# Performance work log

Hardware: AMD Instinct MI355X
Metric: run time of the kernel (lower is better)

Reference implementation:

```python
import jax, jax.numpy as jnp
import numpy as np

B, S, K = 256, 50, 8
D, NH, NL = 512, 8, 2
N_KNOWS, N_PROBS = 1000, 20000
L2 = 2 * NL  # forward layers then backward layers, stacked
HD = D // NH
NEG = -1e9


def _ln(x, g, b, eps=1e-5):
    mu = x.mean(-1, keepdims=True)
    v = ((x - mu) ** 2).mean(-1, keepdims=True)
    return (x - mu) * jax.lax.rsqrt(v + eps) * g + b


def _block(x, m, Wq, bq, Wk, bk, Wv, bv, g1, be1, W1, b1, W2, b2, g2, be2):
    # x: [3B,S,D], m: [3B,1,S,S] additive-OR mask (True = blocked)
    Bx, Sx, Dx = x.shape
    Q = (x @ Wq + bq).reshape(Bx, Sx, NH, HD)
    Kt = (x @ Wk + bk).reshape(Bx, Sx, NH, HD)
    V = (x @ Wv + bv).reshape(Bx, Sx, NH, HD)
    a = jnp.einsum('bqnh,bknh->bnqk', Q, Kt) * (HD ** -0.5)
    a = jnp.where(m, NEG, a)
    p = jax.nn.softmax(a, axis=-1)
    p = jnp.where(m, 0.0, p)  # masked_fill + softmax + where, as in torch source
    o = jnp.einsum('bnqk,bknh->bqnh', p, V).reshape(Bx, Sx, Dx)
    x = _ln(x + o, g1, be1)
    h = jnp.maximum(x @ W1 + b1, 0.0) @ W2 + b2
    return _ln(x + h, g2, be2)


def _forward(probs_his, knows_his, corrs_his, knows_tab, probs_tab, types_tab, pos_tab,
             Wq, bq, Wk, bk, Wv, bv, g1, be1, W1, b1, W2, b2, g2, be2,
             pW1, pb1, pW2, pb2, pW3, pb3):
    info = knows_tab[knows_his].sum(-2) + probs_tab[probs_his] + pos_tab[jnp.arange(S)][None]
    c = corrs_his
    right_t = jnp.where(c, 1, 2)   # corrs==False -> 2
    wrong_t = jnp.where(c, 2, 0)   # corrs==True  -> 2
    norm_t = c.astype(jnp.int32)
    # fold the 3 counterfactual passes (right / wrong / normal) into the batch dim
    x3 = jnp.concatenate([info + types_tab[right_t], info + types_tab[wrong_t], info + types_tab[norm_t]], 0)
    kpm = jnp.tile(probs_his == 0, (3, 1))               # key padding mask [3B,S]
    km = kpm[:, :, None] | kpm[:, None, :]               # OR-combined [3B,S,S]
    tri = jnp.triu(jnp.ones((S, S), bool), 1)
    fm = (tri[None] | km)[:, None]                       # forward (causal) mask
    bm = (tri.T[None] | km)[:, None]                     # backward (anti-causal) mask
    f = x3
    b = x3
    for i in range(NL):
        f = _block(f, fm, Wq[i], bq[i], Wk[i], bk[i], Wv[i], bv[i], g1[i], be1[i], W1[i], b1[i], W2[i], b2[i], g2[i], be2[i])
    for i in range(NL, L2):
        b = _block(b, bm, Wq[i], bq[i], Wk[i], bk[i], Wv[i], bv[i], g1[i], be1[i], W1[i], b1[i], W2[i], b2[i], g2[i], be2[i])
    out = jnp.concatenate([b[:, :1], f[:, :-2] + b[:, 2:], f[:, -1:]], 1)
    h = jnp.concatenate([out, jnp.tile(info, (3, 1, 1))], -1)
    h = jnp.maximum(h @ pW1 + pb1, 0.0)
    h = jnp.maximum(h @ pW2 + pb2, 0.0)
    sc = jax.nn.sigmoid((h @ pW3 + pb3)[..., 0]).reshape(3, B, S)
    # zero out padded positions instead of ragged boolean gather (fixed shape, jit-safe)
    return jnp.where((probs_his > 0)[None], sc, 0.0)


def setup_inputs() -> dict:
    key = jax.random.key(0)
    ks = jax.random.split(key, 16)
    sc = 0.02
    d = {}
    d['probs_his'] = jax.random.randint(ks[0], (B, S), 0, N_PROBS)
    d['knows_his'] = jax.random.randint(ks[1], (B, S, K), 0, N_KNOWS + 1)
    d['corrs_his'] = jax.random.randint(ks[2], (B, S), 0, 2).astype(bool)
    d['knows_tab'] = (jax.random.normal(ks[3], (N_KNOWS + 1, D)) * sc).at[0].set(0.0)  # padding_idx=0
    d['probs_tab'] = (jax.random.normal(ks[4], (N_PROBS + 1, D)) * sc).at[0].set(0.0)
    d['types_tab'] = jax.random.normal(ks[5], (3, D)) * sc
    d['pos_tab'] = jax.random.normal(ks[6], (50, D)) * sc
    d['Wq'] = jax.random.normal(ks[7], (L2, D, D)) * sc
    d['Wk'] = jax.random.normal(ks[8], (L2, D, D)) * sc
    d['Wv'] = jax.random.normal(ks[9], (L2, D, D)) * sc
    d['W1'] = jax.random.normal(ks[10], (L2, D, D)) * sc
    d['W2'] = jax.random.normal(ks[11], (L2, D, D)) * sc
    for n in ('bq', 'bk', 'bv', 'b1', 'b2', 'be1', 'be2'):
        d[n] = jnp.zeros((L2, D))
    d['g1'] = jnp.ones((L2, D))
    d['g2'] = jnp.ones((L2, D))
    d['pW1'] = jax.random.normal(ks[12], (2 * D, D)) * sc
    d['pb1'] = jnp.zeros((D,))
    d['pW2'] = jax.random.normal(ks[13], (D, D // 2)) * sc
    d['pb2'] = jnp.zeros((D // 2,))
    d['pW3'] = jax.random.normal(ks[14], (D // 2, 1)) * sc
    d['pb3'] = jnp.zeros((1,))
    return d


def reference(probs_his, knows_his, corrs_his, knows_tab, probs_tab, types_tab, pos_tab,
              Wq, bq, Wk, bk, Wv, bv, g1, be1, W1, b1, W2, b2, g2, be2,
              pW1, pb1, pW2, pb2, pW3, pb3):
    return _forward(probs_his, knows_his, corrs_his, knows_tab, probs_tab, types_tab, pos_tab,
                    Wq, bq, Wk, bk, Wv, bv, g1, be1, W1, b1, W2, b2, g2, be2,
                    pW1, pb1, pW2, pb2, pW3, pb3)
```

## Files before the change

### kernel.cpp

```cpp
#include <hip/hip_runtime.h>
#include <hip/hip_bf16.h>

#define SEQ 50
#define DD  512
#define NHD 8
#define HDIM 64
#define MPROWS 38400
#define MTROWS 76800

typedef __hip_bfloat16 bf;
typedef __attribute__((ext_vector_type(8))) short bf16x8;
typedef __attribute__((ext_vector_type(4))) float f32x4;

__device__ __forceinline__ float bf2f(unsigned short u) {
    unsigned int x = ((unsigned int)u) << 16;
    return __builtin_bit_cast(float, x);
}
__device__ __forceinline__ unsigned short f2bu(float f) {
    unsigned int u = __builtin_bit_cast(unsigned int, f);
    u += 0x7fffu + ((u >> 16) & 1u);
    return (unsigned short)(u >> 16);
}

#define ASYNC16(g, l) __builtin_amdgcn_global_load_lds( \
    (__attribute__((address_space(1))) void*)(g),       \
    (__attribute__((address_space(3))) void*)(l), 16, 0, 0)

__global__ __launch_bounds__(256) void transpose_cast(
    const float* __restrict__ src, bf* __restrict__ dst,
    int R, int C, size_t sStride, size_t dStride)
{
    __shared__ float tile[32][33];
    int l = blockIdx.z;
    src += (size_t)l * sStride;
    dst += (size_t)l * dStride;
    int c0 = blockIdx.x * 32, r0 = blockIdx.y * 32;
    int tx = threadIdx.x & 31, ty = threadIdx.x >> 5;
    for (int i = ty; i < 32; i += 8)
        tile[i][tx] = src[(size_t)(r0 + i) * C + c0 + tx];
    __syncthreads();
    for (int i = ty; i < 32; i += 8)
        dst[(size_t)(c0 + i) * R + r0 + tx] = __float2bfloat16(tile[tx][i]);
}

__global__ __launch_bounds__(256) void biascat_kernel(
    const float* __restrict__ bq, const float* __restrict__ bk,
    const float* __restrict__ bv, float* __restrict__ out)
{
    int i = blockIdx.x * 256 + threadIdx.x;
    if (i >= 4 * 1536) return;
    int l = i / 1536, c = i % 1536;
    float v;
    if (c < 512)       v = bq[l * 512 + c];
    else if (c < 1024) v = bk[l * 512 + c - 512];
    else               v = bv[l * 512 + c - 1024];
    out[i] = v;
}

__global__ __launch_bounds__(256) void embed_kernel(
    const int* __restrict__ probs_his, const int* __restrict__ knows_his,
    const int* __restrict__ corrs, const float* __restrict__ knows_tab,
    const float* __restrict__ probs_tab, const float* __restrict__ types_tab,
    const float* __restrict__ pos_tab, bf* __restrict__ info, bf* __restrict__ X)
{
    int bs = blockIdx.x * 4 + (threadIdx.x >> 6);
    int lane = threadIdx.x & 63;
    int s = bs % SEQ;
    int p = probs_his[bs];
    int c = corrs[bs];
    int d0 = lane * 8;

    float v[8];
    #pragma unroll
    for (int j = 0; j < 8; ++j)
        v[j] = probs_tab[(size_t)p * DD + d0 + j] + pos_tab[(size_t)s * DD + d0 + j];
    for (int k = 0; k < 8; ++k) {
        int ki = knows_his[bs * 8 + k];
        const float* kr = knows_tab + (size_t)ki * DD + d0;
        #pragma unroll
        for (int j = 0; j < 8; ++j) v[j] += kr[j];
    }
    int t0 = c ? 1 : 2;
    int t1 = c ? 2 : 0;
    int t2 = c ? 1 : 0;
    const float* T0 = types_tab + t0 * DD + d0;
    const float* T1 = types_tab + t1 * DD + d0;
    const float* T2 = types_tab + t2 * DD + d0;
    uint4 xi, x0, x1, x2;
    unsigned short* pi = (unsigned short*)&xi;
    unsigned short* p0 = (unsigned short*)&x0;
    unsigned short* p1 = (unsigned short*)&x1;
    unsigned short* p2 = (unsigned short*)&x2;
    #pragma unroll
    for (int j = 0; j < 8; ++j) {
        pi[j] = f2bu(v[j]);
        p0[j] = f2bu(v[j] + T0[j]);
        p1[j] = f2bu(v[j] + T1[j]);
        p2[j] = f2bu(v[j] + T2[j]);
    }
    size_t base = (size_t)bs * DD + d0;
    const size_t PB = (size_t)12800 * DD;
    *(uint4*)(info + base) = xi;
    *(uint4*)(X + 0 * PB + base) = x0;
    *(uint4*)(X + 1 * PB + base) = x1;
    *(uint4*)(X + 2 * PB + base) = x2;
    *(uint4*)(X + 3 * PB + base) = x0;
    *(uint4*)(X + 4 * PB + base) = x1;
    *(uint4*)(X + 5 * PB + base) = x2;
}

template <int RELU>
__global__ __launch_bounds__(256) void gemm_bt(
    const bf* __restrict__ Ap, const bf* __restrict__ WTp,
    const float* __restrict__ bias, bf* __restrict__ Cp, int N, int Kd, int nN)
{
    __shared__ bf Al[128 * 64];
    __shared__ bf Bl[128 * 64];
    {
    }
    int nwg = gridDim.x;
    int f = blockIdx.x;
    int q8 = nwg >> 3, r8 = nwg & 7;
    int xcd = f & 7, pos = f >> 3;
    int e = (xcd < r8 ? xcd * (q8 + 1) : r8 * (q8 + 1) + (xcd - r8) * q8) + pos;
    int bm = e / nN, bn = e - bm * nN;
    int m0 = bm * 128, n0 = bn * 128;
    int t = threadIdx.x, lane = t & 63, wave = t >> 6;
    int wr = wave >> 1, wc = wave & 1;
    int lr = lane & 15, lg = lane >> 4;

    f32x4 acc[4][4];
    #pragma unroll
    for (int m = 0; m < 4; ++m)
        #pragma unroll
        for (int n = 0; n < 4; ++n)
            acc[m][n] = (f32x4){0.f, 0.f, 0.f, 0.f};

    for (int kt = 0; kt < Kd; kt += 64) {
        #pragma unroll
        for (int i = 0; i < 4; ++i) {
            int c = i * 256 + t;
            int row = c >> 3, col = (c & 7) * 8;
            ASYNC16(Ap  + (size_t)(m0 + row) * Kd + kt + col, Al + c * 8);
            ASYNC16(WTp + (size_t)(n0 + row) * Kd + kt + col, Bl + c * 8);
        }
        __syncthreads();
        #pragma unroll
        for (int kk = 0; kk < 64; kk += 32) {
            int ko = kk + lg * 8;
            bf16x8 af[4], bfr[4];
            #pragma unroll
            for (int m = 0; m < 4; ++m)
                af[m] = *(const bf16x8*)(Al + (wr * 64 + m * 16 + lr) * 64 + ko);
            #pragma unroll
            for (int n = 0; n < 4; ++n)
                bfr[n] = *(const bf16x8*)(Bl + (wc * 64 + n * 16 + lr) * 64 + ko);
            #pragma unroll
            for (int m = 0; m < 4; ++m)
                #pragma unroll
                for (int n = 0; n < 4; ++n)
                    acc[m][n] = __builtin_amdgcn_mfma_f32_16x16x32_bf16(af[m], bfr[n], acc[m][n], 0, 0, 0);
        }
        __syncthreads();
    }
    unsigned short* Cs = (unsigned short*)Cp;
    #pragma unroll
    for (int n = 0; n < 4; ++n) {
        int col = n0 + wc * 64 + n * 16 + lr;
        float bvv = bias[col];
        #pragma unroll
        for (int m = 0; m < 4; ++m) {
            #pragma unroll
            for (int r = 0; r < 4; ++r) {
                int row = m0 + wr * 64 + m * 16 + lg * 4 + r;
                float v = acc[m][n][r] + bvv;
                if (RELU) v = fmaxf(v, 0.f);
                Cs[(size_t)row * N + col] = f2bu(v);
            }
        }
    }
}

__global__ __launch_bounds__(128, 2) void attn_mfma(
    const bf* __restrict__ QKVc, const int* __restrict__ probs_his,
    bf* __restrict__ Oc, int seq0)
{
    __shared__ bf Pl_s[2][4096];
    __shared__ bf Vt_s[2][4096];
    int wave = threadIdx.x >> 6, lane = threadIdx.x & 63;
    bf* Pl = Pl_s[wave];
    bf* Vt = Vt_s[wave];
    int task = blockIdx.x * 2 + wave;
    int h = task & 7, seqL = task >> 3;
    int seqG = seq0 + seqL;
    int st = seqG / 768, b = seqG % 256;
    int lr = lane & 15, kg = lane >> 4;
    const bf* Qb = QKVc + (size_t)seqL * SEQ * 1536 + h * HDIM;
    const bf* Kb = Qb + 512;
    const bf* Vb = Qb + 1024;

    int pvv = (lane < SEQ) ? probs_his[b * SEQ + lane] : 1;
    unsigned long long padm = __ballot(pvv == 0) | 0xFFFC000000000000ull;

    #pragma unroll
    for (int it = 0; it < 8; ++it) {
        int idx = it * 64 + lane;
        int key = idx >> 3, d0 = (idx & 7) * 8;
        uint4 v4 = make_uint4(0u, 0u, 0u, 0u);
        if (key < SEQ) v4 = *(const uint4*)(Vb + (size_t)key * 1536 + d0);
        unsigned short* vs = (unsigned short*)&v4;
        #pragma unroll
        for (int j = 0; j < 8; ++j) {
            int d = d0 + j;
            int byt = (d * 128 + key * 2) ^ ((j & 7) << 4);
            *(unsigned short*)((char*)Vt + byt) = vs[j];
        }
    }

    bf16x8 kf[4][2], qf[4][2];
    #pragma unroll
    for (int m = 0; m < 4; ++m) {
        int rk = 16 * m + lr; if (rk > SEQ - 1) rk = SEQ - 1;
        #pragma unroll
        for (int kb = 0; kb < 2; ++kb) {
            kf[m][kb] = *(const bf16x8*)(Kb + (size_t)rk * 1536 + kb * 32 + kg * 8);
            qf[m][kb] = *(const bf16x8*)(Qb + (size_t)rk * 1536 + kb * 32 + kg * 8);
        }
    }
    f32x4 sacc[4][4];
    #pragma unroll
    for (int m = 0; m < 4; ++m)
        #pragma unroll
        for (int n = 0; n < 4; ++n)
            sacc[m][n] = (f32x4){0.f, 0.f, 0.f, 0.f};
    #pragma unroll
    for (int kb = 0; kb < 2; ++kb)
        #pragma unroll
        for (int m = 0; m < 4; ++m)
            #pragma unroll
            for (int n = 0; n < 4; ++n)
                sacc[m][n] = __builtin_amdgcn_mfma_f32_16x16x32_bf16(kf[m][kb], qf[n][kb], sacc[m][n], 0, 0, 0);

    #pragma unroll
    for (int n = 0; n < 4; ++n) {
        int q = 16 * n + lr;
        int qpad = (int)((padm >> q) & 1ull);
        float p[4][4];
        float mx = -3e38f;
        #pragma unroll
        for (int m = 0; m < 4; ++m)
            #pragma unroll
            for (int r = 0; r < 4; ++r) {
                int key = 16 * m + 4 * kg + r;
                int blocked = qpad | (int)((padm >> key) & 1ull) |
                              (st == 0 ? (key > q) : (key < q));
                float s = sacc[m][n][r] * 0.125f;
                p[m][r] = blocked ? -3e38f : s;
                if (!blocked) mx = fmaxf(mx, s);
            }
        mx = fmaxf(mx, __shfl_xor(mx, 16));
        mx = fmaxf(mx, __shfl_xor(mx, 32));
        float sum = 0.f;
        #pragma unroll
        for (int m = 0; m < 4; ++m)
            #pragma unroll
            for (int r = 0; r < 4; ++r) {
                float e = (p[m][r] > -1e37f) ? __expf(p[m][r] - mx) : 0.f;
                p[m][r] = e;
                sum += e;
            }
        sum += __shfl_xor(sum, 16);
        sum += __shfl_xor(sum, 32);
        float inv = (sum > 0.f) ? 1.f / sum : 0.f;
        #pragma unroll
        for (int m = 0; m < 4; ++m) {
            unsigned int u0 = (unsigned int)f2bu(p[m][0] * inv) |
                              ((unsigned int)f2bu(p[m][1] * inv) << 16);
            unsigned int u1 = (unsigned int)f2bu(p[m][2] * inv) |
                              ((unsigned int)f2bu(p[m][3] * inv) << 16);
            int base = (q * 128 + (16 * m + 4 * kg) * 2) ^ ((q & 7) << 4);
            *(unsigned int*)((char*)Pl + base) = u0;
            *(unsigned int*)((char*)Pl + base + 4) = u1;
        }
    }

    f32x4 oacc[4][4];
    #pragma unroll
    for (int m = 0; m < 4; ++m)
        #pragma unroll
        for (int n = 0; n < 4; ++n)
            oacc[m][n] = (f32x4){0.f, 0.f, 0.f, 0.f};
    #pragma unroll
    for (int kb = 0; kb < 2; ++kb) {
        bf16x8 vf[4], pf[4];
        #pragma unroll
        for (int m = 0; m < 4; ++m) {
            int row = 16 * m + lr;
            int byt = (row * 128 + (kb * 32 + kg * 8) * 2) ^ ((row & 7) << 4);
            vf[m] = *(const bf16x8*)((char*)Vt + byt);
            pf[m] = *(const bf16x8*)((char*)Pl + byt);
        }
        #pragma unroll
        for (int m = 0; m < 4; ++m)
            #pragma unroll
            for (int n = 0; n < 4; ++n)
                oacc[m][n] = __builtin_amdgcn_mfma_f32_16x16x32_bf16(vf[m], pf[n], oacc[m][n], 0, 0, 0);
    }

    #pragma unroll
    for (int n = 0; n < 4; ++n) {
        int q = 16 * n + lr;
        if (q < SEQ) {
            #pragma unroll
            for (int m = 0; m < 4; ++m) {
                uint2 ov;
                ov.x = (unsigned int)f2bu(oacc[m][n][0]) | ((unsigned int)f2bu(oacc[m][n][1]) << 16);
                ov.y = (unsigned int)f2bu(oacc[m][n][2]) | ((unsigned int)f2bu(oacc[m][n][3]) << 16);
                *(uint2*)(Oc + (size_t)(seqL * SEQ + q) * DD + h * HDIM + 16 * m + 4 * kg) = ov;
            }
        }
    }
}

__global__ __launch_bounds__(256) void ln_kernel(
    bf* __restrict__ X, const bf* __restrict__ Rb,
    const float* __restrict__ g, const float* __restrict__ be)
{
    int row = blockIdx.x * 4 + (threadIdx.x >> 6);
    int lane = threadIdx.x & 63;
    uint4 xa = *((const uint4*)(X + (size_t)row * DD) + lane);
    uint4 ra = *((const uint4*)(Rb + (size_t)row * DD) + lane);
    unsigned short* xs = (unsigned short*)&xa;
    unsigned short* rs = (unsigned short*)&ra;
    float v[8];
    float sum = 0.f;
    #pragma unroll
    for (int j = 0; j < 8; ++j) { v[j] = bf2f(xs[j]) + bf2f(rs[j]); sum += v[j]; }
    #pragma unroll
    for (int o = 1; o < 64; o <<= 1) sum += __shfl_xor(sum, o);
    float mu = sum * (1.f / 512.f);
    float ss = 0.f;
    #pragma unroll
    for (int j = 0; j < 8; ++j) { float d = v[j] - mu; ss += d * d; }
    #pragma unroll
    for (int o = 1; o < 64; o <<= 1) ss += __shfl_xor(ss, o);
    float inv = rsqrtf(ss * (1.f / 512.f) + 1e-5f);
    int d0 = lane * 8;
    uint4 ov;
    unsigned short* os = (unsigned short*)&ov;
    #pragma unroll
    for (int j = 0; j < 8; ++j)
        os[j] = f2bu((v[j] - mu) * inv * g[d0 + j] + be[d0 + j]);
    *((uint4*)(X + (size_t)row * DD) + lane) = ov;
}

__global__ __launch_bounds__(256) void combine_kernel(
    const bf* __restrict__ X, const bf* __restrict__ info,
    bf* __restrict__ Hinc, int rh0)
{
    int rl = blockIdx.x * 4 + (threadIdx.x >> 6);
    int rh = rh0 + rl;
    int lane = threadIdx.x & 63;
    int s = rh % SEQ, pb = rh / SEQ, b = pb & 255;
    const size_t MPD = (size_t)MPROWS * DD;
    uint4 o;
    if (s == 0) {
        o = *((const uint4*)(X + MPD + (size_t)(pb * SEQ) * DD) + lane);
    } else if (s == SEQ - 1) {
        o = *((const uint4*)(X + (size_t)(pb * SEQ + SEQ - 1) * DD) + lane);
    } else {
        uint4 a = *((const uint4*)(X + (size_t)(pb * SEQ + s - 1) * DD) + lane);
        uint4 c2 = *((const uint4*)(X + MPD + (size_t)(pb * SEQ + s + 1) * DD) + lane);
        unsigned short* as = (unsigned short*)&a;
        unsigned short* cs = (unsigned short*)&c2;
        unsigned short* os = (unsigned short*)&o;
        #pragma unroll
        for (int j = 0; j < 8; ++j) os[j] = f2bu(bf2f(as[j]) + bf2f(cs[j]));
    }
    uint4 iv = *((const uint4*)(info + (size_t)(b * SEQ + s) * DD) + lane);
    *((uint4*)(Hinc + (size_t)rl * 1024) + lane) = o;
    *((uint4*)(Hinc + (size_t)rl * 1024 + 512) + lane) = iv;
}

__global__ __launch_bounds__(256) void head_final(
    const bf* __restrict__ h2c, const float* __restrict__ pW3,
    const float* __restrict__ pb3, const int* __restrict__ probs_his,
    float* __restrict__ out, int rh0)
{
    int rl = blockIdx.x * 4 + (threadIdx.x >> 6);
    int row = rh0 + rl;
    int lane = threadIdx.x & 63;
    uint2 hv = *((const uint2*)(h2c + (size_t)rl * 256) + lane);
    unsigned short* hs = (unsigned short*)&hv;
    float s = 0.f;
    #pragma unroll
    for (int j = 0; j < 4; ++j) s += bf2f(hs[j]) * pW3[lane * 4 + j];
    #pragma unroll
    for (int o = 1; o < 64; o <<= 1) s += __shfl_xor(s, o);
    if (lane == 0) {
        float logit = s + pb3[0];
        float sc = 1.f / (1.f + __expf(-logit));
        int bb = (row / SEQ) & 255, ss2 = row % SEQ;
        out[row] = (probs_his[bb * SEQ + ss2] > 0) ? sc : 0.f;
    }
}

extern "C" void kernel_launch(void* const* d_in, const int* in_sizes, int n_in,
                              void* d_out, int out_size, void* d_ws, size_t ws_size,
                              hipStream_t stream) {
    const int*   probs_his = (const int*)d_in[0];
    const int*   knows_his = (const int*)d_in[1];
    const int*   corrs     = (const int*)d_in[2];
    const float* knows_tab = (const float*)d_in[3];
    const float* probs_tab = (const float*)d_in[4];
    const float* types_tab = (const float*)d_in[5];
    const float* pos_tab   = (const float*)d_in[6];
    const float* Wq = (const float*)d_in[7];
    const float* Wk = (const float*)d_in[8];
    const float* Wv = (const float*)d_in[9];
    const float* W1 = (const float*)d_in[10];
    const float* W2 = (const float*)d_in[11];
    const float* bq = (const float*)d_in[12];
    const float* bk = (const float*)d_in[13];
    const float* bv = (const float*)d_in[14];
    const float* b1 = (const float*)d_in[15];
    const float* b2 = (const float*)d_in[16];
    const float* be1 = (const float*)d_in[17];
    const float* be2 = (const float*)d_in[18];
    const float* g1 = (const float*)d_in[19];
    const float* g2 = (const float*)d_in[20];
    const float* pW1 = (const float*)d_in[21];
    const float* pb1 = (const float*)d_in[22];
    const float* pW2 = (const float*)d_in[23];
    const float* pb2 = (const float*)d_in[24];
    const float* pW3 = (const float*)d_in[25];
    const float* pb3 = (const float*)d_in[26];

    char* ws = (char*)d_ws;
    bf* WTqkv = (bf*)(ws + 0);
    bf* WT1   = (bf*)(ws + 6291456);
    bf* WT2   = (bf*)(ws + 8388608);
    bf* pW1T  = (bf*)(ws + 10485760);
    bf* pW2T  = (bf*)(ws + 11534336);
    float* bqkv = (float*)(ws + 11796480);
    bf* info  = (bf*)(ws + 11821056);
    bf* X     = (bf*)(ws + 24928256);
    const size_t FIXED = 103571456ull;

    int CR;
    if      (ws_size >= FIXED + (size_t)38400 * 4096) CR = 38400;
    else if (ws_size >= FIXED + (size_t)19200 * 4096) CR = 19200;
    else if (ws_size >= FIXED + (size_t)9600  * 4096) CR = 9600;
    else                                              CR = 3200;

    char* SCR = ws + FIXED;
    bf* QKVc = (bf*)SCR;
    bf* Oc   = (bf*)(SCR + (size_t)CR * 3072);
    bf* F1c  = (bf*)SCR;
    bf* F2c  = (bf*)(SCR + (size_t)CR * 1024);
    bf* Hinc = (bf*)SCR;
    bf* h1c  = (bf*)(SCR + (size_t)CR * 2048);
    bf* h2c  = (bf*)(SCR + (size_t)CR * 3072);

    biascat_kernel<<<dim3(24), dim3(256), 0, stream>>>(bq, bk, bv, bqkv);
    transpose_cast<<<dim3(16,16,4), dim3(256), 0, stream>>>(Wq, WTqkv,          512, 512, 262144, 786432);
    transpose_cast<<<dim3(16,16,4), dim3(256), 0, stream>>>(Wk, WTqkv + 262144, 512, 512, 262144, 786432);
    transpose_cast<<<dim3(16,16,4), dim3(256), 0, stream>>>(Wv, WTqkv + 524288, 512, 512, 262144, 786432);
    transpose_cast<<<dim3(16,16,4), dim3(256), 0, stream>>>(W1, WT1, 512, 512, 262144, 262144);
    transpose_cast<<<dim3(16,16,4), dim3(256), 0, stream>>>(W2, WT2, 512, 512, 262144, 262144);
    transpose_cast<<<dim3(16,32,1), dim3(256), 0, stream>>>(pW1, pW1T, 1024, 512, 0, 0);
    transpose_cast<<<dim3(8,16,1),  dim3(256), 0, stream>>>(pW2, pW2T, 512, 256, 0, 0);
    embed_kernel<<<dim3(3200), dim3(256), 0, stream>>>(probs_his, knows_his, corrs,
        knows_tab, probs_tab, types_tab, pos_tab, info, X);

    const int nck = 38400 / CR;
    const int MT = CR / 128;
    for (int i = 0; i < 2; ++i) {
        for (int hlf = 0; hlf < 2; ++hlf) {
            int lidx = i + 2 * hlf;
            const bf* WTq  = WTqkv + (size_t)lidx * 786432;
            const bf* WT1l = WT1   + (size_t)lidx * 262144;
            const bf* WT2l = WT2   + (size_t)lidx * 262144;
            for (int c = 0; c < nck; ++c) {
                int r0 = hlf * 38400 + c * CR;
                gemm_bt<0><<<dim3(MT * 12), dim3(256), 0, stream>>>(
                    X + (size_t)r0 * DD, WTq, bqkv + lidx * 1536, QKVc, 1536, 512, 12);
                attn_mfma<<<dim3((CR/50) * 4), dim3(128), 0, stream>>>(
                    QKVc, probs_his, Oc, r0 / 50);
                ln_kernel<<<dim3(CR/4), dim3(256), 0, stream>>>(
                    X + (size_t)r0 * DD, Oc, g1 + lidx * DD, be1 + lidx * DD);
            }
            for (int c = 0; c < nck; ++c) {
                int r0 = hlf * 38400 + c * CR;
                gemm_bt<1><<<dim3(MT * 4), dim3(256), 0, stream>>>(
                    X + (size_t)r0 * DD, WT1l, b1 + lidx * DD, F1c, 512, 512, 4);
                gemm_bt<0><<<dim3(MT * 4), dim3(256), 0, stream>>>(
                    F1c, WT2l, b2 + lidx * DD, F2c, 512, 512, 4);
                ln_kernel<<<dim3(CR/4), dim3(256), 0, stream>>>(
                    X + (size_t)r0 * DD, F2c, g2 + lidx * DD, be2 + lidx * DD);
            }
        }
    }

    for (int c = 0; c < nck; ++c) {
        int rh0 = c * CR;
        combine_kernel<<<dim3(CR/4), dim3(256), 0, stream>>>(X, info, Hinc, rh0);
        gemm_bt<1><<<dim3(MT * 4), dim3(256), 0, stream>>>(Hinc, pW1T, pb1, h1c, 512, 1024, 4);
        gemm_bt<1><<<dim3(MT * 2), dim3(256), 0, stream>>>(h1c, pW2T, pb2, h2c, 256, 512, 2);
        head_final<<<dim3(CR/4), dim3(256), 0, stream>>>(h2c, pW3, pb3, probs_his, (float*)d_out, rh0);
    }
}
```

Before: 1.270 ms.

## Replace 128x128 GEMM with double-buffered 256x256 swizzled-LDS GEMM kernel

Replaces the single-buffered 128x128 tile GEMM with a 512-thread kernel computing 256x256 tiles over double-buffered LDS. Global-to-LDS loads for the next k-tiles are issued ahead and overlapped with MFMA work, using explicit vmcnt waits, sched barriers and setprio. An XOR swizzle on LDS columns is added to reduce bank conflicts. The minimum chunk size is raised to 6400 rows so chunks divide into 256-row tiles. The larger tiles give fewer workgroups per launch, which risks underfilling the CUs on small grids, and the 128 KB of LDS limits occupancy to one block per CU.

```diff
diff --git a/kernel.cpp b/kernel.cpp
--- a/kernel.cpp
+++ b/kernel.cpp
@@ -25,6 +25,10 @@
 #define ASYNC16(g, l) __builtin_amdgcn_global_load_lds( \
     (__attribute__((address_space(1))) void*)(g),       \
     (__attribute__((address_space(3))) void*)(l), 16, 0, 0)
+
+#define BARRIER() do { __builtin_amdgcn_sched_barrier(0); \
+    __builtin_amdgcn_s_barrier(); \
+    __builtin_amdgcn_sched_barrier(0); } while (0)
 
 __global__ __launch_bounds__(256) void transpose_cast(
     const float* __restrict__ src, bf* __restrict__ dst,
@@ -110,69 +114,117 @@
 }
 
 template <int RELU>
-__global__ __launch_bounds__(256) void gemm_bt(
+__global__ __launch_bounds__(512, 1) void gemm256(
     const bf* __restrict__ Ap, const bf* __restrict__ WTp,
     const float* __restrict__ bias, bf* __restrict__ Cp, int N, int Kd, int nN)
 {
-    __shared__ bf Al[128 * 64];
-    __shared__ bf Bl[128 * 64];
-    {
-    }
-    int nwg = gridDim.x;
-    int f = blockIdx.x;
+    __shared__ bf As[2][16384];
+    __shared__ bf Bs[2][16384];
+
+    int nwg = gridDim.x, f = blockIdx.x;
     int q8 = nwg >> 3, r8 = nwg & 7;
     int xcd = f & 7, pos = f >> 3;
     int e = (xcd < r8 ? xcd * (q8 + 1) : r8 * (q8 + 1) + (xcd - r8) * q8) + pos;
     int bm = e / nN, bn = e - bm * nN;
-    int m0 = bm * 128, n0 = bn * 128;
+    int m0 = bm * 256, n0 = bn * 256;
     int t = threadIdx.x, lane = t & 63, wave = t >> 6;
-    int wr = wave >> 1, wc = wave & 1;
-    int lr = lane & 15, lg = lane >> 4;
-
-    f32x4 acc[4][4];
-    #pragma unroll
-    for (int m = 0; m < 4; ++m)
+    int wm = wave >> 2, wn = wave & 3;
+    int lr = lane & 15, kg = lane >> 4;
+
+    int srow = t >> 3;
+    int scol = ((t & 7) * 16 ^ ((srow & 7) << 4)) >> 1;
+
+#define STAGE(dbuf, kt) do {                                              \
+    const bf* _as = Ap  + (size_t)(m0 + srow) * Kd + (kt) + scol;         \
+    const bf* _bs = WTp + (size_t)(n0 + srow) * Kd + (kt) + scol;         \
+    _Pragma("unroll")                                                     \
+    for (int _j = 0; _j < 4; ++_j) {                                      \
+        ASYNC16(_as + (size_t)_j * 64 * Kd, As[dbuf] + _j * 4096 + t * 8);\
+        ASYNC16(_bs + (size_t)_j * 64 * Kd, Bs[dbuf] + _j * 4096 + t * 8);\
+    } } while (0)
+
+    int arow = (wm * 128 + lr) * 128;
+    int brow = (wn * 64 + lr) * 128;
+    int colx0 = (kg * 16) ^ ((lr & 7) << 4);
+    int colx1 = (64 + kg * 16) ^ ((lr & 7) << 4);
+
+    f32x4 acc[8][4];
+    #pragma unroll
+    for (int m = 0; m < 8; ++m)
         #pragma unroll
         for (int n = 0; n < 4; ++n)
             acc[m][n] = (f32x4){0.f, 0.f, 0.f, 0.f};
 
-    for (int kt = 0; kt < Kd; kt += 64) {
-        #pragma unroll
-        for (int i = 0; i < 4; ++i) {
-            int c = i * 256 + t;
-            int row = c >> 3, col = (c & 7) * 8;
-            ASYNC16(Ap  + (size_t)(m0 + row) * Kd + kt + col, Al + c * 8);
-            ASYNC16(WTp + (size_t)(n0 + row) * Kd + kt + col, Bl + c * 8);
-        }
-        __syncthreads();
-        #pragma unroll
-        for (int kk = 0; kk < 64; kk += 32) {
-            int ko = kk + lg * 8;
-            bf16x8 af[4], bfr[4];
-            #pragma unroll
-            for (int m = 0; m < 4; ++m)
-                af[m] = *(const bf16x8*)(Al + (wr * 64 + m * 16 + lr) * 64 + ko);
-            #pragma unroll
-            for (int n = 0; n < 4; ++n)
-                bfr[n] = *(const bf16x8*)(Bl + (wc * 64 + n * 16 + lr) * 64 + ko);
-            #pragma unroll
-            for (int m = 0; m < 4; ++m)
+    STAGE(0, 0);
+    STAGE(1, 64);
+    int nt = Kd >> 6;
+    bf16x8 bfrag[4][2];
+
+    for (int tt = 0; tt < nt; ++tt) {
+        int d = tt & 1;
+        const char* Ab = (const char*)As[d];
+        const char* Bb = (const char*)Bs[d];
+        if (tt < nt - 1) asm volatile("s_waitcnt vmcnt(8)" ::: "memory");
+        else             asm volatile("s_waitcnt vmcnt(0)" ::: "memory");
+        BARRIER();
+        {
+            #pragma unroll
+            for (int n = 0; n < 4; ++n) {
+                bfrag[n][0] = *(const bf16x8*)(Bb + brow + n * 2048 + colx0);
+                bfrag[n][1] = *(const bf16x8*)(Bb + brow + n * 2048 + colx1);
+            }
+            bf16x8 af[2][2];
+            #pragma unroll
+            for (int m = 0; m < 2; ++m) {
+                af[m][0] = *(const bf16x8*)(Ab + arow + m * 2048 + colx0);
+                af[m][1] = *(const bf16x8*)(Ab + arow + m * 2048 + colx1);
+            }
+            BARRIER();
+            __builtin_amdgcn_s_setprio(1);
+            #pragma unroll
+            for (int m = 0; m < 2; ++m)
                 #pragma unroll
-                for (int n = 0; n < 4; ++n)
-                    acc[m][n] = __builtin_amdgcn_mfma_f32_16x16x32_bf16(af[m], bfr[n], acc[m][n], 0, 0, 0);
-        }
-        __syncthreads();
-    }
+                for (int n = 0; n < 4; ++n) {
+                    acc[m][n] = __builtin_amdgcn_mfma_f32_16x16x32_bf16(af[m][0], bfrag[n][0], acc[m][n], 0, 0, 0);
+                    acc[m][n] = __builtin_amdgcn_mfma_f32_16x16x32_bf16(af[m][1], bfrag[n][1], acc[m][n], 0, 0, 0);
+                }
+            __builtin_amdgcn_s_setprio(0);
+            BARRIER();
+        }
+        #pragma unroll
+        for (int q = 1; q < 4; ++q) {
+            bf16x8 af[2][2];
+            #pragma unroll
+            for (int m = 0; m < 2; ++m) {
+                af[m][0] = *(const bf16x8*)(Ab + arow + (2 * q + m) * 2048 + colx0);
+                af[m][1] = *(const bf16x8*)(Ab + arow + (2 * q + m) * 2048 + colx1);
+            }
+            BARRIER();
+            __builtin_amdgcn_s_setprio(1);
+            #pragma unroll
+            for (int m = 0; m < 2; ++m)
+                #pragma unroll
+                for (int n = 0; n < 4; ++n) {
+                    acc[2 * q + m][n] = __builtin_amdgcn_mfma_f32_16x16x32_bf16(af[m][0], bfrag[n][0], acc[2 * q + m][n], 0, 0, 0);
+                    acc[2 * q + m][n] = __builtin_amdgcn_mfma_f32_16x16x32_bf16(af[m][1], bfrag[n][1], acc[2 * q + m][n], 0, 0, 0);
+                }
+            __builtin_amdgcn_s_setprio(0);
+            BARRIER();
+        }
+        if (tt + 2 < nt) STAGE(d, (tt + 2) * 64);
+    }
+#undef STAGE
+
     unsigned short* Cs = (unsigned short*)Cp;
     #pragma unroll
     for (int n = 0; n < 4; ++n) {
-        int col = n0 + wc * 64 + n * 16 + lr;
+        int col = n0 + wn * 64 + n * 16 + lr;
         float bvv = bias[col];
         #pragma unroll
-        for (int m = 0; m < 4; ++m) {
+        for (int m = 0; m < 8; ++m) {
             #pragma unroll
             for (int r = 0; r < 4; ++r) {
-                int row = m0 + wr * 64 + m * 16 + lg * 4 + r;
+                int row = m0 + wm * 128 + m * 16 + kg * 4 + r;
                 float v = acc[m][n][r] + bvv;
                 if (RELU) v = fmaxf(v, 0.f);
                 Cs[(size_t)row * N + col] = f2bu(v);
@@ -450,8 +502,7 @@
     int CR;
     if      (ws_size >= FIXED + (size_t)38400 * 4096) CR = 38400;
     else if (ws_size >= FIXED + (size_t)19200 * 4096) CR = 19200;
-    else if (ws_size >= FIXED + (size_t)9600  * 4096) CR = 9600;
-    else                                              CR = 3200;
+    else                                              CR = 6400;
 
     char* SCR = ws + FIXED;
     bf* QKVc = (bf*)SCR;
@@ -474,7 +525,7 @@
         knows_tab, probs_tab, types_tab, pos_tab, info, X);
 
     const int nck = 38400 / CR;
-    const int MT = CR / 128;
+    const int MT = CR / 256;
     for (int i = 0; i < 2; ++i) {
         for (int hlf = 0; hlf < 2; ++hlf) {
             int lidx = i + 2 * hlf;
@@ -483,8 +534,8 @@
             const bf* WT2l = WT2   + (size_t)lidx * 262144;
             for (int c = 0; c < nck; ++c) {
                 int r0 = hlf * 38400 + c * CR;
-                gemm_bt<0><<<dim3(MT * 12), dim3(256), 0, stream>>>(
-                    X + (size_t)r0 * DD, WTq, bqkv + lidx * 1536, QKVc, 1536, 512, 12);
+                gemm256<0><<<dim3(MT * 6), dim3(512), 0, stream>>>(
+                    X + (size_t)r0 * DD, WTq, bqkv + lidx * 1536, QKVc, 1536, 512, 6);
                 attn_mfma<<<dim3((CR/50) * 4), dim3(128), 0, stream>>>(
                     QKVc, probs_his, Oc, r0 / 50);
                 ln_kernel<<<dim3(CR/4), dim3(256), 0, stream>>>(
@@ -492,10 +543,10 @@
             }
             for (int c = 0; c < nck; ++c) {
                 int r0 = hlf * 38400 + c * CR;
-                gemm_bt<1><<<dim3(MT * 4), dim3(256), 0, stream>>>(
-                    X + (size_t)r0 * DD, WT1l, b1 + lidx * DD, F1c, 512, 512, 4);
-                gemm_bt<0><<<dim3(MT * 4), dim3(256), 0, stream>>>(
-                    F1c, WT2l, b2 + lidx * DD, F2c, 512, 512, 4);
+                gemm256<1><<<dim3(MT * 2), dim3(512), 0, stream>>>(
+                    X + (size_t)r0 * DD, WT1l, b1 + lidx * DD, F1c, 512, 512, 2);
+                gemm256<0><<<dim3(MT * 2), dim3(512), 0, stream>>>(
+                    F1c, WT2l, b2 + lidx * DD, F2c, 512, 512, 2);
                 ln_kernel<<<dim3(CR/4), dim3(256), 0, stream>>>(
                     X + (size_t)r0 * DD, F2c, g2 + lidx * DD, be2 + lidx * DD);
             }
@@ -505,8 +556,8 @@
     for (int c = 0; c < nck; ++c) {
         int rh0 = c * CR;
         combine_kernel<<<dim3(CR/4), dim3(256), 0, stream>>>(X, info, Hinc, rh0);
-        gemm_bt<1><<<dim3(MT * 4), dim3(256), 0, stream>>>(Hinc, pW1T, pb1, h1c, 512, 1024, 4);
-        gemm_bt<1><<<dim3(MT * 2), dim3(256), 0, stream>>>(h1c, pW2T, pb2, h2c, 256, 512, 2);
+        gemm256<1><<<dim3(MT * 2), dim3(512), 0, stream>>>(Hinc, pW1T, pb1, h1c, 512, 1024, 2);
+        gemm256<1><<<dim3(MT * 1), dim3(512), 0, stream>>>(h1c, pW2T, pb2, h2c, 256, 512, 1);
         head_final<<<dim3(CR/4), dim3(256), 0, stream>>>(h2c, pW3, pb3, probs_his, (float*)d_out, rh0);
     }
 }
```

New measurement: 1.318 ms. 3.8% more time.

## Factor type embedding out of first-layer QKV projection via linearity

Applied to the files above, without the earlier changes.

For the first layer of each direction, the QKV GEMM runs once on the shared info embedding (12800 rows) rather than on all three counterfactual copies (38400 rows). The type-embedding contribution is projected separately (3 types x 1536 outputs) and added per row according to the corrs-derived type index. This cuts the first-layer QKV GEMM work by about two thirds, at the cost of an extra elementwise add pass and slightly different bf16 rounding. It only applies when the workspace allows the full 38400-row chunk plus room for the small projection table.

```diff
diff --git a/kernel.cpp b/kernel.cpp
--- a/kernel.cpp
+++ b/kernel.cpp
@@ -57,6 +57,50 @@
     out[i] = v;
 }
 
+__global__ __launch_bounds__(256) void tproj_kernel(
+    const float* __restrict__ types_tab, const bf* __restrict__ WTqkv,
+    bf* __restrict__ Tt)
+{
+    int gid = blockIdx.x * 256 + threadIdx.x;
+    if (gid >= 9216) return;
+    int hl = gid / 4608;
+    int t  = (gid / 1536) % 3;
+    int n  = gid % 1536;
+    const unsigned short* w =
+        (const unsigned short*)(WTqkv + (size_t)(hl * 2) * 786432 + (size_t)n * 512);
+    const float* ty = types_tab + t * 512;
+    float a = 0.f;
+    for (int k = 0; k < 512; ++k) a += ty[k] * bf2f(w[k]);
+    Tt[gid] = __float2bfloat16(a);
+}
+
+__global__ __launch_bounds__(256) void qkvadd_kernel(
+    bf* __restrict__ QKVc, const bf* __restrict__ T2,
+    const int* __restrict__ corrs, int rstart)
+{
+    int row = rstart + blockIdx.x * 4 + (threadIdx.x >> 6);
+    int lane = threadIdx.x & 63;
+    int pass = row / 12800;
+    int rr = row % 12800;
+    int c = corrs[rr];
+    int t = (pass == 0) ? (c ? 1 : 2) : (pass == 1) ? (c ? 2 : 0) : (c ? 1 : 0);
+    const bf* src = QKVc + (size_t)rr * 1536 + lane * 8;
+    const bf* tp  = T2 + t * 1536 + lane * 8;
+    bf* dst = QKVc + (size_t)row * 1536 + lane * 8;
+    #pragma unroll
+    for (int j = 0; j < 3; ++j) {
+        uint4 a = *(const uint4*)(src + j * 512);
+        uint4 tb = *(const uint4*)(tp + j * 512);
+        unsigned short* as = (unsigned short*)&a;
+        unsigned short* ts = (unsigned short*)&tb;
+        uint4 o;
+        unsigned short* os = (unsigned short*)&o;
+        #pragma unroll
+        for (int k = 0; k < 8; ++k) os[k] = f2bu(bf2f(as[k]) + bf2f(ts[k]));
+        *(uint4*)(dst + j * 512) = o;
+    }
+}
+
 __global__ __launch_bounds__(256) void embed_kernel(
     const int* __restrict__ probs_his, const int* __restrict__ knows_his,
     const int* __restrict__ corrs, const float* __restrict__ knows_tab,
@@ -116,8 +160,6 @@
 {
     __shared__ bf Al[128 * 64];
     __shared__ bf Bl[128 * 64];
-    {
-    }
     int nwg = gridDim.x;
     int f = blockIdx.x;
     int q8 = nwg >> 3, r8 = nwg & 7;
@@ -453,6 +495,10 @@
     else if (ws_size >= FIXED + (size_t)9600  * 4096) CR = 9600;
     else                                              CR = 3200;
 
+    const int typedOK = (CR == 38400) &&
+        (ws_size >= FIXED + (size_t)38400 * 4096 + 18432);
+    bf* Tt = (bf*)(ws + FIXED + (size_t)38400 * 4096);
+
     char* SCR = ws + FIXED;
     bf* QKVc = (bf*)SCR;
     bf* Oc   = (bf*)(SCR + (size_t)CR * 3072);
@@ -472,6 +518,8 @@
     transpose_cast<<<dim3(8,16,1),  dim3(256), 0, stream>>>(pW2, pW2T, 512, 256, 0, 0);
     embed_kernel<<<dim3(3200), dim3(256), 0, stream>>>(probs_his, knows_his, corrs,
         knows_tab, probs_tab, types_tab, pos_tab, info, X);
+    if (typedOK)
+        tproj_kernel<<<dim3(36), dim3(256), 0, stream>>>(types_tab, WTqkv, Tt);
 
     const int nck = 38400 / CR;
     const int MT = CR / 128;
@@ -483,8 +531,17 @@
             const bf* WT2l = WT2   + (size_t)lidx * 262144;
             for (int c = 0; c < nck; ++c) {
                 int r0 = hlf * 38400 + c * CR;
-                gemm_bt<0><<<dim3(MT * 12), dim3(256), 0, stream>>>(
-                    X + (size_t)r0 * DD, WTq, bqkv + lidx * 1536, QKVc, 1536, 512, 12);
+                if (i == 0 && typedOK) {
+                    gemm_bt<0><<<dim3(100 * 12), dim3(256), 0, stream>>>(
+                        info, WTq, bqkv + lidx * 1536, QKVc, 1536, 512, 12);
+                    qkvadd_kernel<<<dim3(6400), dim3(256), 0, stream>>>(
+                        QKVc, Tt + hlf * 4608, corrs, 12800);
+                    qkvadd_kernel<<<dim3(3200), dim3(256), 0, stream>>>(
+                        QKVc, Tt + hlf * 4608, corrs, 0);
+                } else {
+                    gemm_bt<0><<<dim3(MT * 12), dim3(256), 0, stream>>>(
+                        X + (size_t)r0 * DD, WTq, bqkv + lidx * 1536, QKVc, 1536, 512, 12);
+                }
                 attn_mfma<<<dim3((CR/50) * 4), dim3(128), 0, stream>>>(
                     QKVc, probs_his, Oc, r0 / 50);
                 ln_kernel<<<dim3(CR/4), dim3(256), 0, stream>>>(
```

After: 1.243 ms. -2.2%, faster.

## Exploit linearity to share layer-0 QKV and head info projection across passes

Applied to the files above, without the earlier changes.

For the first layer the three counterfactual inputs differ only by a type embedding, so the QKV projection is computed once on the shared info rows and the projected type vectors are added per pass in the epilogue, cutting that GEMM's M dimension by three. The head's info half of pW1 is likewise projected once and added in a fused epilogue. FFN GEMMs and LayerNorms for forward and backward halves are merged into single launches with per-half weight selection. This needs extra workspace and a full-scratch path, and the type projection rounds to bf16 separately, which slightly changes numerics.

```diff
diff --git a/kernel.cpp b/kernel.cpp
--- a/kernel.cpp
+++ b/kernel.cpp
@@ -57,6 +57,23 @@
     out[i] = v;
 }
 
+__global__ __launch_bounds__(256) void tproj_kernel(
+    const float* __restrict__ types_tab, const bf* __restrict__ WTqkv,
+    bf* __restrict__ Tt)
+{
+    int gid = blockIdx.x * 256 + threadIdx.x;
+    if (gid >= 9216) return;
+    int hl = gid / 4608;
+    int t  = (gid / 1536) % 3;
+    int n  = gid % 1536;
+    const unsigned short* w =
+        (const unsigned short*)(WTqkv + (size_t)(hl * 2) * 786432 + (size_t)n * 512);
+    const float* ty = types_tab + t * 512;
+    float a = 0.f;
+    for (int k = 0; k < 512; ++k) a += ty[k] * bf2f(w[k]);
+    Tt[gid] = __float2bfloat16(a);
+}
+
 __global__ __launch_bounds__(256) void embed_kernel(
     const int* __restrict__ probs_his, const int* __restrict__ knows_his,
     const int* __restrict__ corrs, const float* __restrict__ knows_tab,
@@ -111,13 +128,87 @@
 
 template <int RELU>
 __global__ __launch_bounds__(256) void gemm_bt(
-    const bf* __restrict__ Ap, const bf* __restrict__ WTp,
-    const float* __restrict__ bias, bf* __restrict__ Cp, int N, int Kd, int nN)
+    const bf* __restrict__ Ap, const bf* __restrict__ WT0, const bf* __restrict__ WT1,
+    const float* __restrict__ bias0, const float* __restrict__ bias1,
+    bf* __restrict__ Cp, int N, int Kd, int nN, int mtHalf)
 {
     __shared__ bf Al[128 * 64];
     __shared__ bf Bl[128 * 64];
-    {
-    }
+    int nwg = gridDim.x;
+    int f = blockIdx.x;
+    int q8 = nwg >> 3, r8 = nwg & 7;
+    int xcd = f & 7, pos = f >> 3;
+    int e = (xcd < r8 ? xcd * (q8 + 1) : r8 * (q8 + 1) + (xcd - r8) * q8) + pos;
+    int bm = e / nN, bn = e - bm * nN;
+    const bf* WTp;
+    const float* bias;
+    if (bm < mtHalf) { WTp = WT0; bias = bias0; }
+    else             { WTp = WT1; bias = bias1; }
+    int m0 = bm * 128, n0 = bn * 128;
+    int t = threadIdx.x, lane = t & 63, wave = t >> 6;
+    int wr = wave >> 1, wc = wave & 1;
+    int lr = lane & 15, lg = lane >> 4;
+
+    f32x4 acc[4][4];
+    #pragma unroll
+    for (int m = 0; m < 4; ++m)
+        #pragma unroll
+        for (int n = 0; n < 4; ++n)
+            acc[m][n] = (f32x4){0.f, 0.f, 0.f, 0.f};
+
+    for (int kt = 0; kt < Kd; kt += 64) {
+        #pragma unroll
+        for (int i = 0; i < 4; ++i) {
+            int c = i * 256 + t;
+            int row = c >> 3, col = (c & 7) * 8;
+            ASYNC16(Ap  + (size_t)(m0 + row) * Kd + kt + col, Al + c * 8);
+            ASYNC16(WTp + (size_t)(n0 + row) * Kd + kt + col, Bl + c * 8);
+        }
+        __syncthreads();
+        #pragma unroll
+        for (int kk = 0; kk < 64; kk += 32) {
+            int ko = kk + lg * 8;
+            bf16x8 af[4], bfr[4];
+            #pragma unroll
+            for (int m = 0; m < 4; ++m)
+                af[m] = *(const bf16x8*)(Al + (wr * 64 + m * 16 + lr) * 64 + ko);
+            #pragma unroll
+            for (int n = 0; n < 4; ++n)
+                bfr[n] = *(const bf16x8*)(Bl + (wc * 64 + n * 16 + lr) * 64 + ko);
+            #pragma unroll
+            for (int m = 0; m < 4; ++m)
+                #pragma unroll
+                for (int n = 0; n < 4; ++n)
+                    acc[m][n] = __builtin_amdgcn_mfma_f32_16x16x32_bf16(af[m], bfr[n], acc[m][n], 0, 0, 0);
+        }
+        __syncthreads();
+    }
+    unsigned short* Cs = (unsigned short*)Cp;
+    #pragma unroll
+    for (int n = 0; n < 4; ++n) {
+        int col = n0 + wc * 64 + n * 16 + lr;
+        float bvv = bias[col];
+        #pragma unroll
+        for (int m = 0; m < 4; ++m) {
+            #pragma unroll
+            for (int r = 0; r < 4; ++r) {
+                int row = m0 + wr * 64 + m * 16 + lg * 4 + r;
+                float v = acc[m][n][r] + bvv;
+                if (RELU) v = fmaxf(v, 0.f);
+                Cs[(size_t)row * N + col] = f2bu(v);
+            }
+        }
+    }
+}
+
+__global__ __launch_bounds__(256) void gemm_l0(
+    const bf* __restrict__ Ap, const bf* __restrict__ WTp,
+    const float* __restrict__ bias, const bf* __restrict__ Tth,
+    const int* __restrict__ corrs, bf* __restrict__ QKVc)
+{
+    __shared__ bf Al[128 * 64];
+    __shared__ bf Bl[128 * 64];
+    const int nN = 12, Kd = 512, N = 1536;
     int nwg = gridDim.x;
     int f = blockIdx.x;
     int q8 = nwg >> 3, r8 = nwg & 7;
@@ -163,18 +254,99 @@
         }
         __syncthreads();
     }
-    unsigned short* Cs = (unsigned short*)Cp;
+    unsigned short* Cs = (unsigned short*)QKVc;
+    const unsigned short* Tu = (const unsigned short*)Tth;
     #pragma unroll
     for (int n = 0; n < 4; ++n) {
         int col = n0 + wc * 64 + n * 16 + lr;
         float bvv = bias[col];
+        float T0c = bf2f(Tu[0 * 1536 + col]);
+        float T1c = bf2f(Tu[1 * 1536 + col]);
+        float T2c = bf2f(Tu[2 * 1536 + col]);
         #pragma unroll
         for (int m = 0; m < 4; ++m) {
             #pragma unroll
             for (int r = 0; r < 4; ++r) {
                 int row = m0 + wr * 64 + m * 16 + lg * 4 + r;
+                int c = corrs[row];
                 float v = acc[m][n][r] + bvv;
-                if (RELU) v = fmaxf(v, 0.f);
+                float tv0 = c ? T1c : T2c;
+                float tv1 = c ? T2c : T0c;
+                float tv2 = c ? T1c : T0c;
+                size_t b0 = (size_t)row * N + col;
+                Cs[b0]                         = f2bu(v + tv0);
+                Cs[b0 + (size_t)12800 * N]     = f2bu(v + tv1);
+                Cs[b0 + (size_t)25600 * N]     = f2bu(v + tv2);
+            }
+        }
+    }
+}
+
+__global__ __launch_bounds__(256) void gemm_head(
+    const bf* __restrict__ Ap, const bf* __restrict__ WTp,
+    const bf* __restrict__ IPp, bf* __restrict__ Cp, int nN)
+{
+    __shared__ bf Al[128 * 64];
+    __shared__ bf Bl[128 * 64];
+    const int Kd = 512, N = 512;
+    int nwg = gridDim.x;
+    int f = blockIdx.x;
+    int q8 = nwg >> 3, r8 = nwg & 7;
+    int xcd = f & 7, pos = f >> 3;
+    int e = (xcd < r8 ? xcd * (q8 + 1) : r8 * (q8 + 1) + (xcd - r8) * q8) + pos;
+    int bm = e / nN, bn = e - bm * nN;
+    int m0 = bm * 128, n0 = bn * 128;
+    int t = threadIdx.x, lane = t & 63, wave = t >> 6;
+    int wr = wave >> 1, wc = wave & 1;
+    int lr = lane & 15, lg = lane >> 4;
+
+    f32x4 acc[4][4];
+    #pragma unroll
+    for (int m = 0; m < 4; ++m)
+        #pragma unroll
+        for (int n = 0; n < 4; ++n)
+            acc[m][n] = (f32x4){0.f, 0.f, 0.f, 0.f};
+
+    for (int kt = 0; kt < Kd; kt += 64) {
+        #pragma unroll
+        for (int i = 0; i < 4; ++i) {
+            int c = i * 256 + t;
+            int row = c >> 3, col = (c & 7) * 8;
+            ASYNC16(Ap  + (size_t)(m0 + row) * Kd + kt + col, Al + c * 8);
+            ASYNC16(WTp + (size_t)(n0 + row) * Kd + kt + col, Bl + c * 8);
+        }
+        __syncthreads();
+        #pragma unroll
+        for (int kk = 0; kk < 64; kk += 32) {
+            int ko = kk + lg * 8;
+            bf16x8 af[4], bfr[4];
+            #pragma unroll
+            for (int m = 0; m < 4; ++m)
+                af[m] = *(const bf16x8*)(Al + (wr * 64 + m * 16 + lr) * 64 + ko);
+            #pragma unroll
+            for (int n = 0; n < 4; ++n)
+                bfr[n] = *(const bf16x8*)(Bl + (wc * 64 + n * 16 + lr) * 64 + ko);
+            #pragma unroll
+            for (int m = 0; m < 4; ++m)
+                #pragma unroll
+                for (int n = 0; n < 4; ++n)
+                    acc[m][n] = __builtin_amdgcn_mfma_f32_16x16x32_bf16(af[m], bfr[n], acc[m][n], 0, 0, 0);
+        }
+        __syncthreads();
+    }
+    unsigned short* Cs = (unsigned short*)Cp;
+    const unsigned short* IPu = (const unsigned short*)IPp;
+    #pragma unroll
+    for (int n = 0; n < 4; ++n) {
+        int col = n0 + wc * 64 + n * 16 + lr;
+        #pragma unroll
+        for (int m = 0; m < 4; ++m) {
+            #pragma unroll
+            for (int r = 0; r < 4; ++r) {
+                int row = m0 + wr * 64 + m * 16 + lg * 4 + r;
+                int rr = row % 12800;
+                float v = acc[m][n][r] + bf2f(IPu[(size_t)rr * 512 + col]);
+                v = fmaxf(v, 0.f);
                 Cs[(size_t)row * N + col] = f2bu(v);
             }
         }
@@ -324,10 +496,14 @@
 
 __global__ __launch_bounds__(256) void ln_kernel(
     bf* __restrict__ X, const bf* __restrict__ Rb,
-    const float* __restrict__ g, const float* __restrict__ be)
+    const float* __restrict__ g_all, const float* __restrict__ be_all,
+    int lf, int lb)
 {
     int row = blockIdx.x * 4 + (threadIdx.x >> 6);
     int lane = threadIdx.x & 63;
+    int layer = (row < MPROWS) ? lf : lb;
+    const float* g = g_all + layer * DD;
+    const float* be = be_all + layer * DD;
     uint4 xa = *((const uint4*)(X + (size_t)row * DD) + lane);
     uint4 ra = *((const uint4*)(Rb + (size_t)row * DD) + lane);
     unsigned short* xs = (unsigned short*)&xa;
@@ -356,7 +532,7 @@
 
 __global__ __launch_bounds__(256) void combine_kernel(
     const bf* __restrict__ X, const bf* __restrict__ info,
-    bf* __restrict__ Hinc, int rh0)
+    bf* __restrict__ Hinc, int rh0, int hstride, int withInfo)
 {
     int rl = blockIdx.x * 4 + (threadIdx.x >> 6);
     int rh = rh0 + rl;
@@ -377,9 +553,11 @@
         #pragma unroll
         for (int j = 0; j < 8; ++j) os[j] = f2bu(bf2f(as[j]) + bf2f(cs[j]));
     }
-    uint4 iv = *((const uint4*)(info + (size_t)(b * SEQ + s) * DD) + lane);
-    *((uint4*)(Hinc + (size_t)rl * 1024) + lane) = o;
-    *((uint4*)(Hinc + (size_t)rl * 1024 + 512) + lane) = iv;
+    *((uint4*)(Hinc + (size_t)rl * hstride) + lane) = o;
+    if (withInfo) {
+        uint4 iv = *((const uint4*)(info + (size_t)(b * SEQ + s) * DD) + lane);
+        *((uint4*)(Hinc + (size_t)rl * hstride + 512) + lane) = iv;
+    }
 }
 
 __global__ __launch_bounds__(256) void head_final(
@@ -441,19 +619,92 @@
     bf* WT1   = (bf*)(ws + 6291456);
     bf* WT2   = (bf*)(ws + 8388608);
     bf* pW1T  = (bf*)(ws + 10485760);
-    bf* pW2T  = (bf*)(ws + 11534336);
-    float* bqkv = (float*)(ws + 11796480);
-    bf* info  = (bf*)(ws + 11821056);
-    bf* X     = (bf*)(ws + 24928256);
-    const size_t FIXED = 103571456ull;
+    bf* pW1aT = (bf*)(ws + 11534336);
+    bf* pW1bT = (bf*)(ws + 12058624);
+    bf* pW2T  = (bf*)(ws + 12582912);
+    float* bqkv = (float*)(ws + 12845056);
+    bf* info  = (bf*)(ws + 12869632);
+    bf* X     = (bf*)(ws + 25976832);
+    const size_t FIXED = 104620032ull;
+    const size_t FULLSCR = (size_t)38400 * 4096;
 
     int CR;
-    if      (ws_size >= FIXED + (size_t)38400 * 4096) CR = 38400;
-    else if (ws_size >= FIXED + (size_t)19200 * 4096) CR = 19200;
-    else if (ws_size >= FIXED + (size_t)9600  * 4096) CR = 9600;
-    else                                              CR = 3200;
+    if      (ws_size >= FIXED + FULLSCR)                  CR = 38400;
+    else if (ws_size >= FIXED + (size_t)19200 * 4096)     CR = 19200;
+    else if (ws_size >= FIXED + (size_t)9600  * 4096)     CR = 9600;
+    else                                                  CR = 3200;
+    const int full = (CR == 38400) &&
+        (ws_size >= FIXED + FULLSCR + 18432);
+    bf* Tt = (bf*)(ws + FIXED + FULLSCR);
 
     char* SCR = ws + FIXED;
+
+    biascat_kernel<<<dim3(24), dim3(256), 0, stream>>>(bq, bk, bv, bqkv);
+    transpose_cast<<<dim3(16,16,4), dim3(256), 0, stream>>>(Wq, WTqkv,          512, 512, 262144, 786432);
+    transpose_cast<<<dim3(16,16,4), dim3(256), 0, stream>>>(Wk, WTqkv + 262144, 512, 512, 262144, 786432);
+    transpose_cast<<<dim3(16,16,4), dim3(256), 0, stream>>>(Wv, WTqkv + 524288, 512, 512, 262144, 786432);
+    transpose_cast<<<dim3(16,16,4), dim3(256), 0, stream>>>(W1, WT1, 512, 512, 262144, 262144);
+    transpose_cast<<<dim3(16,16,4), dim3(256), 0, stream>>>(W2, WT2, 512, 512, 262144, 262144);
+    transpose_cast<<<dim3(16,32,1), dim3(256), 0, stream>>>(pW1, pW1T, 1024, 512, 0, 0);
+    transpose_cast<<<dim3(16,16,1), dim3(256), 0, stream>>>(pW1, pW1aT, 512, 512, 0, 0);
+    transpose_cast<<<dim3(16,16,1), dim3(256), 0, stream>>>(pW1 + 262144, pW1bT, 512, 512, 0, 0);
+    transpose_cast<<<dim3(8,16,1),  dim3(256), 0, stream>>>(pW2, pW2T, 512, 256, 0, 0);
+    embed_kernel<<<dim3(3200), dim3(256), 0, stream>>>(probs_his, knows_his, corrs,
+        knows_tab, probs_tab, types_tab, pos_tab, info, X);
+    if (full)
+        tproj_kernel<<<dim3(36), dim3(256), 0, stream>>>(types_tab, WTqkv, Tt);
+
+    const int BIG = 1 << 30;
+
+    if (full) {
+        bf* QKVc = (bf*)SCR;
+        bf* Oc   = (bf*)(SCR + (size_t)38400 * 3072);
+        bf* F1c  = (bf*)SCR;
+        bf* F2c  = (bf*)(SCR + (size_t)76800 * 1024);
+        bf* Hin  = (bf*)SCR;
+        bf* h1c  = (bf*)(SCR + 39321600);
+        bf* h2c  = (bf*)(SCR + 78643200);
+        bf* IPb  = (bf*)(SCR + 98304000);
+
+        for (int i = 0; i < 2; ++i) {
+            for (int hlf = 0; hlf < 2; ++hlf) {
+                int lidx = i + 2 * hlf;
+                bf* Xh = X + (size_t)hlf * 38400 * DD;
+                if (i == 0) {
+                    gemm_l0<<<dim3(1200), dim3(256), 0, stream>>>(
+                        info, WTqkv + (size_t)lidx * 786432, bqkv + lidx * 1536,
+                        Tt + hlf * 4608, corrs, QKVc);
+                } else {
+                    gemm_bt<0><<<dim3(3600), dim3(256), 0, stream>>>(
+                        Xh, WTqkv + (size_t)lidx * 786432, WTqkv + (size_t)lidx * 786432,
+                        bqkv + lidx * 1536, bqkv + lidx * 1536, QKVc, 1536, 512, 12, BIG);
+                }
+                attn_mfma<<<dim3(3072), dim3(128), 0, stream>>>(
+                    QKVc, probs_his, Oc, hlf * 768);
+                ln_kernel<<<dim3(9600), dim3(256), 0, stream>>>(
+                    Xh, Oc, g1, be1, lidx, lidx);
+            }
+            gemm_bt<1><<<dim3(2400), dim3(256), 0, stream>>>(
+                X, WT1 + (size_t)i * 262144, WT1 + (size_t)(i + 2) * 262144,
+                b1 + i * 512, b1 + (i + 2) * 512, F1c, 512, 512, 4, 300);
+            gemm_bt<0><<<dim3(2400), dim3(256), 0, stream>>>(
+                F1c, WT2 + (size_t)i * 262144, WT2 + (size_t)(i + 2) * 262144,
+                b2 + i * 512, b2 + (i + 2) * 512, F2c, 512, 512, 4, 300);
+            ln_kernel<<<dim3(19200), dim3(256), 0, stream>>>(
+                X, F2c, g2, be2, i, i + 2);
+        }
+
+        combine_kernel<<<dim3(9600), dim3(256), 0, stream>>>(X, info, Hin, 0, 512, 0);
+        gemm_bt<0><<<dim3(400), dim3(256), 0, stream>>>(
+            info, pW1bT, pW1bT, pb1, pb1, IPb, 512, 512, 4, BIG);
+        gemm_head<<<dim3(1200), dim3(256), 0, stream>>>(Hin, pW1aT, IPb, h1c, 4);
+        gemm_bt<1><<<dim3(600), dim3(256), 0, stream>>>(
+            h1c, pW2T, pW2T, pb2, pb2, h2c, 256, 512, 2, BIG);
+        head_final<<<dim3(9600), dim3(256), 0, stream>>>(
+            h2c, pW3, pb3, probs_his, (float*)d_out, 0);
+        return;
+    }
+
     bf* QKVc = (bf*)SCR;
     bf* Oc   = (bf*)(SCR + (size_t)CR * 3072);
     bf* F1c  = (bf*)SCR;
@@ -461,17 +712,6 @@
     bf* Hinc = (bf*)SCR;
     bf* h1c  = (bf*)(SCR + (size_t)CR * 2048);
     bf* h2c  = (bf*)(SCR + (size_t)CR * 3072);
-
-    biascat_kernel<<<dim3(24), dim3(256), 0, stream>>>(bq, bk, bv, bqkv);
-    transpose_cast<<<dim3(16,16,4), dim3(256), 0, stream>>>(Wq, WTqkv,          512, 512, 262144, 786432);
-    transpose_cast<<<dim3(16,16,4), dim3(256), 0, stream>>>(Wk, WTqkv + 262144, 512, 512, 262144, 786432);
-    transpose_cast<<<dim3(16,16,4), dim3(256), 0, stream>>>(Wv, WTqkv + 524288, 512, 512, 262144, 786432);
-    transpose_cast<<<dim3(16,16,4), dim3(256), 0, stream>>>(W1, WT1, 512, 512, 262144, 262144);
-    transpose_cast<<<dim3(16,16,4), dim3(256), 0, stream>>>(W2, WT2, 512, 512, 262144, 262144);
-    transpose_cast<<<dim3(16,32,1), dim3(256), 0, stream>>>(pW1, pW1T, 1024, 512, 0, 0);
-    transpose_cast<<<dim3(8,16,1),  dim3(256), 0, stream>>>(pW2, pW2T, 512, 256, 0, 0);
-    embed_kernel<<<dim3(3200), dim3(256), 0, stream>>>(probs_his, knows_his, corrs,
-        knows_tab, probs_tab, types_tab, pos_tab, info, X);
 
     const int nck = 38400 / CR;
     const int MT = CR / 128;
@@ -484,29 +724,34 @@
             for (int c = 0; c < nck; ++c) {
                 int r0 = hlf * 38400 + c * CR;
                 gemm_bt<0><<<dim3(MT * 12), dim3(256), 0, stream>>>(
-                    X + (size_t)r0 * DD, WTq, bqkv + lidx * 1536, QKVc, 1536, 512, 12);
+                    X + (size_t)r0 * DD, WTq, WTq, bqkv + lidx * 1536,
+                    bqkv + lidx * 1536, QKVc, 1536, 512, 12, BIG);
                 attn_mfma<<<dim3((CR/50) * 4), dim3(128), 0, stream>>>(
                     QKVc, probs_his, Oc, r0 / 50);
                 ln_kernel<<<dim3(CR/4), dim3(256), 0, stream>>>(
-                    X + (size_t)r0 * DD, Oc, g1 + lidx * DD, be1 + lidx * DD);
+                    X + (size_t)r0 * DD, Oc, g1, be1, lidx, lidx);
             }
             for (int c = 0; c < nck; ++c) {
                 int r0 = hlf * 38400 + c * CR;
                 gemm_bt<1><<<dim3(MT * 4), dim3(256), 0, stream>>>(
-                    X + (size_t)r0 * DD, WT1l, b1 + lidx * DD, F1c, 512, 512, 4);
+                    X + (size_t)r0 * DD, WT1l, WT1l, b1 + lidx * 512,
+                    b1 + lidx * 512, F1c, 512, 512, 4, BIG);
                 gemm_bt<0><<<dim3(MT * 4), dim3(256), 0, stream>>>(
-                    F1c, WT2l, b2 + lidx * DD, F2c, 512, 512, 4);
+                    F1c, WT2l, WT2l, b2 + lidx * 512, b2 + lidx * 512,
+                    F2c, 512, 512, 4, BIG);
                 ln_kernel<<<dim3(CR/4), dim3(256), 0, stream>>>(
-                    X + (size_t)r0 * DD, F2c, g2 + lidx * DD, be2 + lidx * DD);
-            }
-        }
-    }
-
+                    X + (size_t)r0 * DD, F2c, g2, be2, lidx, lidx);
+            }
+        }
+    }
     for (int c = 0; c < nck; ++c) {
         int rh0 = c * CR;
-        combine_kernel<<<dim3(CR/4), dim3(256), 0, stream>>>(X, info, Hinc, rh0);
-        gemm_bt<1><<<dim3(MT * 4), dim3(256), 0, stream>>>(Hinc, pW1T, pb1, h1c, 512, 1024, 4);
-        gemm_bt<1><<<dim3(MT * 2), dim3(256), 0, stream>>>(h1c, pW2T, pb2, h2c, 256, 512, 2);
-        head_final<<<dim3(CR/4), dim3(256), 0, stream>>>(h2c, pW3, pb3, probs_his, (float*)d_out, rh0);
-    }
-}
+        combine_kernel<<<dim3(CR/4), dim3(256), 0, stream>>>(X, info, Hinc, rh0, 1024, 1);
+        gemm_bt<1><<<dim3(MT * 4), dim3(256), 0, stream>>>(
+            Hinc, pW1T, pW1T, pb1, pb1, h1c, 512, 1024, 4, BIG);
+        gemm_bt<1><<<dim3(MT * 2), dim3(256), 0, stream>>>(
+            h1c, pW2T, pW2T, pb2, pb2, h2c, 256, 512, 2, BIG);
+        head_final<<<dim3(CR/4), dim3(256), 0, stream>>>(
+            h2c, pW3, pb3, probs_his, (float*)d_out, rh0);
+    }
+}
```

Result: faster. 1.155 ms (-9.1%).
